# Performance work log

Measured on AMD Instinct MI355X. Metric: run time of the kernel, lower is better.

Reference implementation:

```python
import jax, jax.numpy as jnp
import numpy as np
import jax.lax as lax

B, S, E, H = 8, 4096, 1024, 128
TAU = 1.0
MIN_K = 32

def setup_inputs() -> dict:
    key = jax.random.key(0)
    k0, k1, k2, k3 = jax.random.split(key, 4)
    token_embeddings = jax.random.normal(k0, (B, S, E), dtype=jnp.float32)
    w1 = jax.random.normal(k1, (E, H), dtype=jnp.float32) * (1.0 / np.sqrt(E))
    b1 = jnp.zeros((H,), dtype=jnp.float32)
    w2 = jax.random.normal(k2, (H, 1), dtype=jnp.float32) * (1.0 / np.sqrt(H))
    b2 = jnp.zeros((1,), dtype=jnp.float32)
    # uniform noise for Gumbel, same bounds as the original module
    u = jax.random.uniform(k3, (B, S), minval=1e-08, maxval=1.0 - 1e-08, dtype=jnp.float32)
    return {"token_embeddings": token_embeddings, "w1": w1, "b1": b1, "w2": w2, "b2": b2, "u": u}

def reference(token_embeddings, w1, b1, w2, b2, u):
    # scorer MLP: Dense(H) -> relu -> Dense(1), squeeze -> [B, S]
    h = jax.nn.relu(jnp.einsum('bse,eh->bsh', token_embeddings, w1) + b1)
    importance_logits = (jnp.einsum('bsh,ho->bso', h, w2) + b2)[..., 0]  # [B, S]

    # expected_k (value_function is None): soft count of kept tokens
    expected_k = jax.nn.sigmoid(importance_logits).sum(axis=-1)  # [B]
    k = jnp.clip(expected_k.astype(jnp.int32), MIN_K, None)      # [B]

    # Gumbel-softmax top-k, hard=True
    gumbel = -jnp.log(-jnp.log(u))
    soft_mask = jax.nn.softmax((importance_logits + gumbel) / TAU, axis=-1)  # [B, S]

    # hard mask: 1.0 at the top-k[i] positions of soft_mask per row.
    # Equivalent to the original argsort + while_loop scatter: positions with
    # descending-sort rank < k[i] get 1.0.
    order = jnp.argsort(-soft_mask, axis=-1)          # [B, S] descending order
    ranks = jnp.argsort(order, axis=-1)               # rank of each position
    hard_mask = (ranks < k[:, None]).astype(soft_mask.dtype)

    selection_mask = lax.stop_gradient(hard_mask - soft_mask) + soft_mask
    filtered_embeddings = token_embeddings * selection_mask[..., None]
    return filtered_embeddings, selection_mask, expected_k
```

## Files before the change

kernel.cpp:

```cpp
#include <hip/hip_runtime.h>
#include <hip/hip_bf16.h>
#include <math.h>

#define B_ 8
#define S_ 4096
#define E_ 1024
#define H_ 128
#define MIN_K 32
#define OUT_MASK_OFF (B_*S_*E_)
#define OUT_EK_OFF   (B_*S_*E_ + B_*S_)

#define LOGITS_OFF 0
#define SOFT_OFF   131072
#define CNT_OFF    262144
#define KROW_OFF   393216
#define W1T_HI_OFF 393248
#define W1T_LO_OFF 655392

typedef __attribute__((ext_vector_type(8))) short   frag8;
typedef __attribute__((ext_vector_type(4))) float   fragc;
typedef __attribute__((ext_vector_type(4))) unsigned short us4;

static __device__ __forceinline__ unsigned short bf16_rne(float f) {
  unsigned u = __float_as_uint(f);
  unsigned r = u + 0x7FFF + ((u >> 16) & 1);
  return (unsigned short)(r >> 16);
}
static __device__ __forceinline__ float bf16_to_f32(unsigned short h) {
  return __uint_as_float(((unsigned)h) << 16);
}

__global__ __launch_bounds__(256) void prep_w_kernel(
    const float* __restrict__ w1,
    unsigned short* __restrict__ w1t_hi, unsigned short* __restrict__ w1t_lo)
{
  int id = blockIdx.x * 256 + threadIdx.x;
  int k  = id >> 5;
  int n4 = id & 31;
  float4 w = *(const float4*)(w1 + k * H_ + n4 * 4);
#pragma unroll
  for (int e = 0; e < 4; ++e) {
    float f = (e == 0) ? w.x : (e == 1) ? w.y : (e == 2) ? w.z : w.w;
    unsigned short hi = bf16_rne(f);
    unsigned short lo = bf16_rne(f - bf16_to_f32(hi));
    int n = n4 * 4 + e;
    w1t_hi[n * E_ + k] = hi;
    w1t_lo[n * E_ + k] = lo;
  }
}

#define KT 32
#define XS_STRIDE 40

__global__ __launch_bounds__(256) void scorer_kernel(
    const float* __restrict__ x,
    const unsigned short* __restrict__ w1t_hi,
    const unsigned short* __restrict__ w1t_lo,
    const float* __restrict__ b1, const float* __restrict__ w2,
    const float* __restrict__ b2, float* __restrict__ logits)
{
  __shared__ unsigned short xs_hi[64 * XS_STRIDE];
  __shared__ unsigned short xs_lo[64 * XS_STRIDE];
  __shared__ float part[4][64];

  const int tid  = threadIdx.x;
  const int wave = tid >> 6;
  const int lane = tid & 63;
  const int l15  = lane & 15;
  const int quad = lane >> 4;
  const int m0   = blockIdx.x * 64;
  const int nbase = wave * 32;

  fragc acc[4][2];
#pragma unroll
  for (int mt = 0; mt < 4; ++mt)
#pragma unroll
    for (int nt = 0; nt < 2; ++nt)
      acc[mt][nt] = (fragc)(0.f);

  const int sm0 = tid >> 3, skq0 = tid & 7;
  const int sm1 = (tid + 256) >> 3, skq1 = (tid + 256) & 7;

  float4 p0 = *(const float4*)(x + (size_t)(m0 + sm0) * E_ + skq0 * 4);
  float4 p1 = *(const float4*)(x + (size_t)(m0 + sm1) * E_ + skq1 * 4);

  for (int k0 = 0; k0 < E_; k0 += KT) {
    __syncthreads();
    {
      us4 h4, l4;
      float fv[4] = {p0.x, p0.y, p0.z, p0.w};
#pragma unroll
      for (int e = 0; e < 4; ++e) {
        unsigned short hi = bf16_rne(fv[e]);
        h4[e] = hi; l4[e] = bf16_rne(fv[e] - bf16_to_f32(hi));
      }
      *(us4*)&xs_hi[sm0 * XS_STRIDE + skq0 * 4] = h4;
      *(us4*)&xs_lo[sm0 * XS_STRIDE + skq0 * 4] = l4;
      float gv[4] = {p1.x, p1.y, p1.z, p1.w};
#pragma unroll
      for (int e = 0; e < 4; ++e) {
        unsigned short hi = bf16_rne(gv[e]);
        h4[e] = hi; l4[e] = bf16_rne(gv[e] - bf16_to_f32(hi));
      }
      *(us4*)&xs_hi[sm1 * XS_STRIDE + skq1 * 4] = h4;
      *(us4*)&xs_lo[sm1 * XS_STRIDE + skq1 * 4] = l4;
    }
    __syncthreads();

    if (k0 + KT < E_) {
      p0 = *(const float4*)(x + (size_t)(m0 + sm0) * E_ + (k0 + KT) + skq0 * 4);
      p1 = *(const float4*)(x + (size_t)(m0 + sm1) * E_ + (k0 + KT) + skq1 * 4);
    }

    frag8 ah[4], al[4];
#pragma unroll
    for (int mt = 0; mt < 4; ++mt) {
      int a = (mt * 16 + l15) * XS_STRIDE + quad * 8;
      ah[mt] = *(const frag8*)&xs_hi[a];
      al[mt] = *(const frag8*)&xs_lo[a];
    }
    frag8 bh[2], bl[2];
#pragma unroll
    for (int nt = 0; nt < 2; ++nt) {
      int n = nbase + nt * 16 + l15;
      size_t off = (size_t)n * E_ + k0 + quad * 8;
      bh[nt] = *(const frag8*)(w1t_hi + off);
      bl[nt] = *(const frag8*)(w1t_lo + off);
    }
#pragma unroll
    for (int mt = 0; mt < 4; ++mt)
#pragma unroll
      for (int nt = 0; nt < 2; ++nt) {
        acc[mt][nt] = __builtin_amdgcn_mfma_f32_16x16x32_bf16(ah[mt], bh[nt], acc[mt][nt], 0, 0, 0);
        acc[mt][nt] = __builtin_amdgcn_mfma_f32_16x16x32_bf16(ah[mt], bl[nt], acc[mt][nt], 0, 0, 0);
        acc[mt][nt] = __builtin_amdgcn_mfma_f32_16x16x32_bf16(al[mt], bh[nt], acc[mt][nt], 0, 0, 0);
      }
  }

  float b1v[2], w2v[2];
#pragma unroll
  for (int nt = 0; nt < 2; ++nt) {
    int n = nbase + nt * 16 + l15;
    b1v[nt] = b1[n]; w2v[nt] = w2[n];
  }
  float v[4][4];
#pragma unroll
  for (int mt = 0; mt < 4; ++mt)
#pragma unroll
    for (int reg = 0; reg < 4; ++reg) {
      float p = 0.f;
#pragma unroll
      for (int nt = 0; nt < 2; ++nt) {
        float h = acc[mt][nt][reg] + b1v[nt];
        h = h > 0.f ? h : 0.f;
        p = fmaf(h, w2v[nt], p);
      }
      v[mt][reg] = p;
    }
#pragma unroll
  for (int mask = 1; mask < 16; mask <<= 1)
#pragma unroll
    for (int mt = 0; mt < 4; ++mt)
#pragma unroll
      for (int reg = 0; reg < 4; ++reg)
        v[mt][reg] += __shfl_xor(v[mt][reg], mask);

  if (l15 == 0) {
#pragma unroll
    for (int mt = 0; mt < 4; ++mt)
#pragma unroll
      for (int reg = 0; reg < 4; ++reg)
        part[wave][mt * 16 + quad * 4 + reg] = v[mt][reg];
  }
  __syncthreads();
  if (tid < 64)
    logits[m0 + tid] = ((part[0][tid] + part[1][tid]) + (part[2][tid] + part[3][tid])) + b2[0];
}

__global__ __launch_bounds__(1024) void row_kernel(
    const float* __restrict__ logits, const float* __restrict__ u,
    float* __restrict__ soft, int* __restrict__ krow, float* __restrict__ ek_out)
{
  const int b = blockIdx.x;
  const int t = threadIdx.x;
  const float* Lrow = logits + b * S_;
  const float* urow = u + b * S_;

  __shared__ double red[1024];
  __shared__ float  redf[1024];

  float z[4];
  double psig = 0.0;
  float zmax = -INFINITY;
#pragma unroll
  for (int i = 0; i < 4; ++i) {
    int j = t + i * 1024;
    float L = Lrow[j];
    float g = -logf(-logf(urow[j]));
    z[i] = L + g;
    psig += (double)(1.f / (1.f + expf(-L)));
    zmax = fmaxf(zmax, z[i]);
  }
  red[t] = psig; redf[t] = zmax;
  __syncthreads();
  for (int s2 = 512; s2 > 0; s2 >>= 1) {
    if (t < s2) { red[t] += red[t + s2]; redf[t] = fmaxf(redf[t], redf[t + s2]); }
    __syncthreads();
  }
  __shared__ float m_sh; __shared__ double ek_sh;
  if (t == 0) { m_sh = redf[0]; ek_sh = red[0]; }
  __syncthreads();
  float m = m_sh;

  float e[4];
  double pexp = 0.0;
#pragma unroll
  for (int i = 0; i < 4; ++i) { e[i] = expf(z[i] - m); pexp += (double)e[i]; }
  red[t] = pexp;
  __syncthreads();
  for (int s2 = 512; s2 > 0; s2 >>= 1) {
    if (t < s2) red[t] += red[t + s2];
    __syncthreads();
  }
  __shared__ float den_sh;
  if (t == 0) den_sh = (float)red[0];
  __syncthreads();
  float den = den_sh;
#pragma unroll
  for (int i = 0; i < 4; ++i) soft[b * S_ + t + i * 1024] = e[i] / den;

  if (t == 0) {
    float ekf = (float)ek_sh;
    int k = (int)ekf;
    if (k < MIN_K) k = MIN_K;
    krow[b] = k;
    ek_out[b] = ekf;
  }
}

__global__ __launch_bounds__(256) void rank_kernel(
    const float* __restrict__ soft, int* __restrict__ counts)
{
  __shared__ float4 sjs[256];
  const int b  = blockIdx.z;
  const int ic = blockIdx.x;
  const int jc = blockIdx.y;
  const int tid = threadIdx.x;
  const float* row = soft + b * S_;

  sjs[tid] = ((const float4*)row)[jc * 256 + tid];
  const int i = ic * 256 + tid;
  const float si = row[i];
  __syncthreads();

  int cnt = 0;
  const int jbase = jc * 1024;
  for (int j4 = 0; j4 < 256; ++j4) {
    float4 vv = sjs[j4];
    int j = jbase + j4 * 4;
    cnt += (vv.x > si) || (vv.x == si && (j + 0) < i);
    cnt += (vv.y > si) || (vv.y == si && (j + 1) < i);
    cnt += (vv.z > si) || (vv.z == si && (j + 2) < i);
    cnt += (vv.w > si) || (vv.w == si && (j + 3) < i);
  }
  atomicAdd(&counts[b * S_ + i], cnt);
}

__global__ __launch_bounds__(256) void filter_kernel(
    const float* __restrict__ x, const float* __restrict__ soft,
    const int* __restrict__ counts, const int* __restrict__ krow,
    float* __restrict__ out, float* __restrict__ mask_out)
{
  const int token = blockIdx.x;
  const int b = token >> 12;
  const float s = soft[token];
  const float h = (counts[token] < krow[b]) ? 1.f : 0.f;
  const float sel = (h - s) + s;

  size_t base = (size_t)token * (E_ / 4) + threadIdx.x;
  float4 v = ((const float4*)x)[base];
  v.x *= sel; v.y *= sel; v.z *= sel; v.w *= sel;
  ((float4*)out)[base] = v;
  if (threadIdx.x == 0) mask_out[token] = sel;
}

extern "C" void kernel_launch(void* const* d_in, const int* in_sizes, int n_in,
                              void* d_out, int out_size, void* d_ws, size_t ws_size,
                              hipStream_t stream) {
  const float* x  = (const float*)d_in[0];
  const float* w1 = (const float*)d_in[1];
  const float* b1 = (const float*)d_in[2];
  const float* w2 = (const float*)d_in[3];
  const float* b2 = (const float*)d_in[4];
  const float* u  = (const float*)d_in[5];

  float* out = (float*)d_out;
  float* out_filt = out;
  float* out_mask = out + OUT_MASK_OFF;
  float* out_ek   = out + OUT_EK_OFF;

  char* ws = (char*)d_ws;
  float*          ws_logits = (float*)(ws + LOGITS_OFF);
  float*          ws_soft   = (float*)(ws + SOFT_OFF);
  int*            ws_cnt    = (int*)(ws + CNT_OFF);
  int*            ws_krow   = (int*)(ws + KROW_OFF);
  unsigned short* ws_w1thi  = (unsigned short*)(ws + W1T_HI_OFF);
  unsigned short* ws_w1tlo  = (unsigned short*)(ws + W1T_LO_OFF);

  hipMemsetAsync(ws_cnt, 0, B_ * S_ * sizeof(int), stream);
  prep_w_kernel<<<dim3(128), dim3(256), 0, stream>>>(w1, ws_w1thi, ws_w1tlo);
  scorer_kernel<<<dim3(B_ * S_ / 64), dim3(256), 0, stream>>>(
      x, ws_w1thi, ws_w1tlo, b1, w2, b2, ws_logits);
  row_kernel<<<dim3(B_), dim3(1024), 0, stream>>>(ws_logits, u, ws_soft, ws_krow, out_ek);
  rank_kernel<<<dim3(16, 4, 8), dim3(256), 0, stream>>>(ws_soft, ws_cnt);
  filter_kernel<<<dim3(B_ * S_), dim3(256), 0, stream>>>(
      x, ws_soft, ws_cnt, ws_krow, out_filt, out_mask);
}
```

Measured before the change: 319.1 us.

## Retile scorer GEMM with LDS-staged weights, fuse gumbel/partials, skip zero-mask loads

The scorer now computes 128-token tiles, with the split-bf16 weights staged in LDS and a 2x2 wave layout, so each weight load is reused across more tokens. Its epilogue now computes the Gumbel-perturbed logits plus per-64-token partial sums of the sigmoid and the max. That leaves the row kernel with only a small reduction and shuffle-based softmax sums. The filter kernel skips reading x for tokens whose selection value is exactly zero and writes zeros instead. The tradeoffs are fewer scorer blocks (256), more LDS per block, and a different floating-point summation order for expected_k.

```diff
diff --git a/kernel.cpp b/kernel.cpp
--- a/kernel.cpp
+++ b/kernel.cpp
@@ -10,12 +10,14 @@
 #define OUT_MASK_OFF (B_*S_*E_)
 #define OUT_EK_OFF   (B_*S_*E_ + B_*S_)
 
-#define LOGITS_OFF 0
+#define Z_OFF      0
 #define SOFT_OFF   131072
 #define CNT_OFF    262144
 #define KROW_OFF   393216
-#define W1T_HI_OFF 393248
-#define W1T_LO_OFF 655392
+#define PARTS_OFF  393248
+#define PARTM_OFF  397344
+#define W1T_HI_OFF 399392
+#define W1T_LO_OFF 661536
 
 typedef __attribute__((ext_vector_type(8))) short   frag8;
 typedef __attribute__((ext_vector_type(4))) float   fragc;
@@ -50,17 +52,21 @@
 }
 
 #define KT 32
-#define XS_STRIDE 40
+#define LDST 40
 
 __global__ __launch_bounds__(256) void scorer_kernel(
     const float* __restrict__ x,
     const unsigned short* __restrict__ w1t_hi,
     const unsigned short* __restrict__ w1t_lo,
     const float* __restrict__ b1, const float* __restrict__ w2,
-    const float* __restrict__ b2, float* __restrict__ logits)
-{
-  __shared__ unsigned short xs_hi[64 * XS_STRIDE];
-  __shared__ unsigned short xs_lo[64 * XS_STRIDE];
+    const float* __restrict__ b2, const float* __restrict__ u,
+    float* __restrict__ zout, double* __restrict__ partS,
+    float* __restrict__ partM)
+{
+  __shared__ unsigned short xs_hi[128 * LDST];
+  __shared__ unsigned short xs_lo[128 * LDST];
+  __shared__ unsigned short bs_hi[128 * LDST];
+  __shared__ unsigned short bs_lo[128 * LDST];
   __shared__ float part[4][64];
 
   const int tid  = threadIdx.x;
@@ -68,162 +74,190 @@
   const int lane = tid & 63;
   const int l15  = lane & 15;
   const int quad = lane >> 4;
-  const int m0   = blockIdx.x * 64;
-  const int nbase = wave * 32;
-
-  fragc acc[4][2];
-#pragma unroll
-  for (int mt = 0; mt < 4; ++mt)
-#pragma unroll
-    for (int nt = 0; nt < 2; ++nt)
-      acc[mt][nt] = (fragc)(0.f);
-
-  const int sm0 = tid >> 3, skq0 = tid & 7;
-  const int sm1 = (tid + 256) >> 3, skq1 = (tid + 256) & 7;
-
-  float4 p0 = *(const float4*)(x + (size_t)(m0 + sm0) * E_ + skq0 * 4);
-  float4 p1 = *(const float4*)(x + (size_t)(m0 + sm1) * E_ + skq1 * 4);
+  const int wr   = wave >> 1;
+  const int wc   = wave & 1;
+  const int m0   = blockIdx.x * 128;
+
+  fragc acc[4][4];
+#pragma unroll
+  for (int i = 0; i < 4; ++i)
+#pragma unroll
+    for (int j = 0; j < 4; ++j) acc[i][j] = (fragc)(0.f);
+
+  int sm[4], skq[4];
+#pragma unroll
+  for (int i = 0; i < 4; ++i) { int idx = tid + i * 256; sm[i] = idx >> 3; skq[i] = idx & 7; }
+  int bn[2], bkq[2];
+#pragma unroll
+  for (int i = 0; i < 2; ++i) { int idx = tid + i * 256; bn[i] = idx >> 2; bkq[i] = idx & 3; }
+
+  float4 p[4];
+  uint4  qh[2], ql[2];
+#pragma unroll
+  for (int i = 0; i < 4; ++i)
+    p[i] = *(const float4*)(x + (size_t)(m0 + sm[i]) * E_ + skq[i] * 4);
+#pragma unroll
+  for (int i = 0; i < 2; ++i) {
+    size_t off = (size_t)bn[i] * E_ + bkq[i] * 8;
+    qh[i] = *(const uint4*)(w1t_hi + off);
+    ql[i] = *(const uint4*)(w1t_lo + off);
+  }
 
   for (int k0 = 0; k0 < E_; k0 += KT) {
     __syncthreads();
-    {
+#pragma unroll
+    for (int i = 0; i < 4; ++i) {
       us4 h4, l4;
-      float fv[4] = {p0.x, p0.y, p0.z, p0.w};
+      float fv[4] = {p[i].x, p[i].y, p[i].z, p[i].w};
 #pragma unroll
       for (int e = 0; e < 4; ++e) {
         unsigned short hi = bf16_rne(fv[e]);
         h4[e] = hi; l4[e] = bf16_rne(fv[e] - bf16_to_f32(hi));
       }
-      *(us4*)&xs_hi[sm0 * XS_STRIDE + skq0 * 4] = h4;
-      *(us4*)&xs_lo[sm0 * XS_STRIDE + skq0 * 4] = l4;
-      float gv[4] = {p1.x, p1.y, p1.z, p1.w};
-#pragma unroll
-      for (int e = 0; e < 4; ++e) {
-        unsigned short hi = bf16_rne(gv[e]);
-        h4[e] = hi; l4[e] = bf16_rne(gv[e] - bf16_to_f32(hi));
+      *(us4*)&xs_hi[sm[i] * LDST + skq[i] * 4] = h4;
+      *(us4*)&xs_lo[sm[i] * LDST + skq[i] * 4] = l4;
+    }
+#pragma unroll
+    for (int i = 0; i < 2; ++i) {
+      *(uint4*)&bs_hi[bn[i] * LDST + bkq[i] * 8] = qh[i];
+      *(uint4*)&bs_lo[bn[i] * LDST + bkq[i] * 8] = ql[i];
+    }
+    __syncthreads();
+
+    if (k0 + KT < E_) {
+#pragma unroll
+      for (int i = 0; i < 4; ++i)
+        p[i] = *(const float4*)(x + (size_t)(m0 + sm[i]) * E_ + (k0 + KT) + skq[i] * 4);
+#pragma unroll
+      for (int i = 0; i < 2; ++i) {
+        size_t off = (size_t)bn[i] * E_ + (k0 + KT) + bkq[i] * 8;
+        qh[i] = *(const uint4*)(w1t_hi + off);
+        ql[i] = *(const uint4*)(w1t_lo + off);
       }
-      *(us4*)&xs_hi[sm1 * XS_STRIDE + skq1 * 4] = h4;
-      *(us4*)&xs_lo[sm1 * XS_STRIDE + skq1 * 4] = l4;
-    }
-    __syncthreads();
-
-    if (k0 + KT < E_) {
-      p0 = *(const float4*)(x + (size_t)(m0 + sm0) * E_ + (k0 + KT) + skq0 * 4);
-      p1 = *(const float4*)(x + (size_t)(m0 + sm1) * E_ + (k0 + KT) + skq1 * 4);
-    }
-
-    frag8 ah[4], al[4];
-#pragma unroll
-    for (int mt = 0; mt < 4; ++mt) {
-      int a = (mt * 16 + l15) * XS_STRIDE + quad * 8;
-      ah[mt] = *(const frag8*)&xs_hi[a];
-      al[mt] = *(const frag8*)&xs_lo[a];
-    }
-    frag8 bh[2], bl[2];
-#pragma unroll
-    for (int nt = 0; nt < 2; ++nt) {
-      int n = nbase + nt * 16 + l15;
-      size_t off = (size_t)n * E_ + k0 + quad * 8;
-      bh[nt] = *(const frag8*)(w1t_hi + off);
-      bl[nt] = *(const frag8*)(w1t_lo + off);
-    }
-#pragma unroll
-    for (int mt = 0; mt < 4; ++mt)
-#pragma unroll
-      for (int nt = 0; nt < 2; ++nt) {
-        acc[mt][nt] = __builtin_amdgcn_mfma_f32_16x16x32_bf16(ah[mt], bh[nt], acc[mt][nt], 0, 0, 0);
-        acc[mt][nt] = __builtin_amdgcn_mfma_f32_16x16x32_bf16(ah[mt], bl[nt], acc[mt][nt], 0, 0, 0);
-        acc[mt][nt] = __builtin_amdgcn_mfma_f32_16x16x32_bf16(al[mt], bh[nt], acc[mt][nt], 0, 0, 0);
+    }
+
+    frag8 bh[4], bl[4];
+#pragma unroll
+    for (int ntl = 0; ntl < 4; ++ntl) {
+      int a = ((wc * 4 + ntl) * 16 + l15) * LDST + quad * 8;
+      bh[ntl] = *(const frag8*)&bs_hi[a];
+      bl[ntl] = *(const frag8*)&bs_lo[a];
+    }
+#pragma unroll
+    for (int mtl = 0; mtl < 4; ++mtl) {
+      int a = ((wr * 4 + mtl) * 16 + l15) * LDST + quad * 8;
+      frag8 ah = *(const frag8*)&xs_hi[a];
+      frag8 al = *(const frag8*)&xs_lo[a];
+#pragma unroll
+      for (int ntl = 0; ntl < 4; ++ntl) {
+        acc[mtl][ntl] = __builtin_amdgcn_mfma_f32_16x16x32_bf16(ah, bh[ntl], acc[mtl][ntl], 0, 0, 0);
+        acc[mtl][ntl] = __builtin_amdgcn_mfma_f32_16x16x32_bf16(ah, bl[ntl], acc[mtl][ntl], 0, 0, 0);
+        acc[mtl][ntl] = __builtin_amdgcn_mfma_f32_16x16x32_bf16(al, bh[ntl], acc[mtl][ntl], 0, 0, 0);
       }
-  }
-
-  float b1v[2], w2v[2];
-#pragma unroll
-  for (int nt = 0; nt < 2; ++nt) {
-    int n = nbase + nt * 16 + l15;
-    b1v[nt] = b1[n]; w2v[nt] = w2[n];
+    }
+  }
+
+  float b1v[4], w2v[4];
+#pragma unroll
+  for (int ntl = 0; ntl < 4; ++ntl) {
+    int n = (wc * 4 + ntl) * 16 + l15;
+    b1v[ntl] = b1[n]; w2v[ntl] = w2[n];
   }
   float v[4][4];
 #pragma unroll
-  for (int mt = 0; mt < 4; ++mt)
+  for (int mtl = 0; mtl < 4; ++mtl)
 #pragma unroll
     for (int reg = 0; reg < 4; ++reg) {
-      float p = 0.f;
-#pragma unroll
-      for (int nt = 0; nt < 2; ++nt) {
-        float h = acc[mt][nt][reg] + b1v[nt];
+      float pv = 0.f;
+#pragma unroll
+      for (int ntl = 0; ntl < 4; ++ntl) {
+        float h = acc[mtl][ntl][reg] + b1v[ntl];
         h = h > 0.f ? h : 0.f;
-        p = fmaf(h, w2v[nt], p);
+        pv = fmaf(h, w2v[ntl], pv);
       }
-      v[mt][reg] = p;
+      v[mtl][reg] = pv;
     }
 #pragma unroll
   for (int mask = 1; mask < 16; mask <<= 1)
 #pragma unroll
-    for (int mt = 0; mt < 4; ++mt)
+    for (int mtl = 0; mtl < 4; ++mtl)
 #pragma unroll
       for (int reg = 0; reg < 4; ++reg)
-        v[mt][reg] += __shfl_xor(v[mt][reg], mask);
+        v[mtl][reg] += __shfl_xor(v[mtl][reg], mask);
 
   if (l15 == 0) {
 #pragma unroll
-    for (int mt = 0; mt < 4; ++mt)
+    for (int mtl = 0; mtl < 4; ++mtl)
 #pragma unroll
       for (int reg = 0; reg < 4; ++reg)
-        part[wave][mt * 16 + quad * 4 + reg] = v[mt][reg];
-  }
-  __syncthreads();
-  if (tid < 64)
-    logits[m0 + tid] = ((part[0][tid] + part[1][tid]) + (part[2][tid] + part[3][tid])) + b2[0];
-}
-
-__global__ __launch_bounds__(1024) void row_kernel(
-    const float* __restrict__ logits, const float* __restrict__ u,
-    float* __restrict__ soft, int* __restrict__ krow, float* __restrict__ ek_out)
+        part[wave][mtl * 16 + quad * 4 + reg] = v[mtl][reg];
+  }
+  __syncthreads();
+
+  if (tid < 128) {
+    const int wgrp = tid >> 6;
+    const int token = m0 + tid;
+    float L = part[wgrp * 2][tid & 63] + part[wgrp * 2 + 1][tid & 63] + b2[0];
+    float g = -logf(-logf(u[token]));
+    float z = L + g;
+    zout[token] = z;
+    double s = (double)(1.f / (1.f + expf(-L)));
+    float zm = z;
+#pragma unroll
+    for (int mask = 1; mask < 64; mask <<= 1) {
+      s += __shfl_xor(s, mask);
+      zm = fmaxf(zm, __shfl_xor(zm, mask));
+    }
+    if ((tid & 63) == 0) {
+      int pidx = blockIdx.x * 2 + wgrp;
+      partS[pidx] = s;
+      partM[pidx] = zm;
+    }
+  }
+}
+
+__global__ __launch_bounds__(1024) void softmax_kernel(
+    const float* __restrict__ z, const double* __restrict__ partS,
+    const float* __restrict__ partM, float* __restrict__ soft,
+    int* __restrict__ krow, float* __restrict__ ek_out)
 {
   const int b = blockIdx.x;
   const int t = threadIdx.x;
-  const float* Lrow = logits + b * S_;
-  const float* urow = u + b * S_;
-
-  __shared__ double red[1024];
-  __shared__ float  redf[1024];
-
-  float z[4];
-  double psig = 0.0;
-  float zmax = -INFINITY;
+  __shared__ float m_sh;
+  __shared__ double ek_sh;
+  __shared__ double wp[16];
+  __shared__ float den_sh;
+
+  if (t < 64) {
+    double ps = partS[b * 64 + t];
+    float  pm = partM[b * 64 + t];
+#pragma unroll
+    for (int mask = 1; mask < 64; mask <<= 1) {
+      ps += __shfl_xor(ps, mask);
+      pm = fmaxf(pm, __shfl_xor(pm, mask));
+    }
+    if (t == 0) { ek_sh = ps; m_sh = pm; }
+  }
+  __syncthreads();
+  float m = m_sh;
+
+  float e[4];
+  double pe = 0.0;
 #pragma unroll
   for (int i = 0; i < 4; ++i) {
-    int j = t + i * 1024;
-    float L = Lrow[j];
-    float g = -logf(-logf(urow[j]));
-    z[i] = L + g;
-    psig += (double)(1.f / (1.f + expf(-L)));
-    zmax = fmaxf(zmax, z[i]);
-  }
-  red[t] = psig; redf[t] = zmax;
-  __syncthreads();
-  for (int s2 = 512; s2 > 0; s2 >>= 1) {
-    if (t < s2) { red[t] += red[t + s2]; redf[t] = fmaxf(redf[t], redf[t + s2]); }
-    __syncthreads();
-  }
-  __shared__ float m_sh; __shared__ double ek_sh;
-  if (t == 0) { m_sh = redf[0]; ek_sh = red[0]; }
-  __syncthreads();
-  float m = m_sh;
-
-  float e[4];
-  double pexp = 0.0;
-#pragma unroll
-  for (int i = 0; i < 4; ++i) { e[i] = expf(z[i] - m); pexp += (double)e[i]; }
-  red[t] = pexp;
-  __syncthreads();
-  for (int s2 = 512; s2 > 0; s2 >>= 1) {
-    if (t < s2) red[t] += red[t + s2];
-    __syncthreads();
-  }
-  __shared__ float den_sh;
-  if (t == 0) den_sh = (float)red[0];
+    e[i] = expf(z[b * S_ + t + i * 1024] - m);
+    pe += (double)e[i];
+  }
+#pragma unroll
+  for (int mask = 1; mask < 64; mask <<= 1) pe += __shfl_xor(pe, mask);
+  if ((t & 63) == 0) wp[t >> 6] = pe;
+  __syncthreads();
+  if (t < 16) {
+    double vv = wp[t];
+#pragma unroll
+    for (int mask = 1; mask < 16; mask <<= 1) vv += __shfl_xor(vv, mask);
+    if (t == 0) den_sh = (float)vv;
+  }
   __syncthreads();
   float den = den_sh;
 #pragma unroll
@@ -278,9 +312,13 @@
   const float sel = (h - s) + s;
 
   size_t base = (size_t)token * (E_ / 4) + threadIdx.x;
-  float4 v = ((const float4*)x)[base];
-  v.x *= sel; v.y *= sel; v.z *= sel; v.w *= sel;
-  ((float4*)out)[base] = v;
+  if (sel == 0.f) {
+    ((float4*)out)[base] = make_float4(0.f, 0.f, 0.f, 0.f);
+  } else {
+    float4 v = ((const float4*)x)[base];
+    v.x *= sel; v.y *= sel; v.z *= sel; v.w *= sel;
+    ((float4*)out)[base] = v;
+  }
   if (threadIdx.x == 0) mask_out[token] = sel;
 }
 
@@ -300,18 +338,21 @@
   float* out_ek   = out + OUT_EK_OFF;
 
   char* ws = (char*)d_ws;
-  float*          ws_logits = (float*)(ws + LOGITS_OFF);
+  float*          ws_z      = (float*)(ws + Z_OFF);
   float*          ws_soft   = (float*)(ws + SOFT_OFF);
   int*            ws_cnt    = (int*)(ws + CNT_OFF);
   int*            ws_krow   = (int*)(ws + KROW_OFF);
+  double*         ws_partS  = (double*)(ws + PARTS_OFF);
+  float*          ws_partM  = (float*)(ws + PARTM_OFF);
   unsigned short* ws_w1thi  = (unsigned short*)(ws + W1T_HI_OFF);
   unsigned short* ws_w1tlo  = (unsigned short*)(ws + W1T_LO_OFF);
 
   hipMemsetAsync(ws_cnt, 0, B_ * S_ * sizeof(int), stream);
   prep_w_kernel<<<dim3(128), dim3(256), 0, stream>>>(w1, ws_w1thi, ws_w1tlo);
-  scorer_kernel<<<dim3(B_ * S_ / 64), dim3(256), 0, stream>>>(
-      x, ws_w1thi, ws_w1tlo, b1, w2, b2, ws_logits);
-  row_kernel<<<dim3(B_), dim3(1024), 0, stream>>>(ws_logits, u, ws_soft, ws_krow, out_ek);
+  scorer_kernel<<<dim3(B_ * S_ / 128), dim3(256), 0, stream>>>(
+      x, ws_w1thi, ws_w1tlo, b1, w2, b2, u, ws_z, ws_partS, ws_partM);
+  softmax_kernel<<<dim3(B_), dim3(1024), 0, stream>>>(
+      ws_z, ws_partS, ws_partM, ws_soft, ws_krow, out_ek);
   rank_kernel<<<dim3(16, 4, 8), dim3(256), 0, stream>>>(ws_soft, ws_cnt);
   filter_kernel<<<dim3(B_ * S_), dim3(256), 0, stream>>>(
       x, ws_soft, ws_cnt, ws_krow, out_filt, out_mask);
```

After: 346.4 us. +8.6%, slower.
